# Optimization experiments

Measured on AMD Instinct MI355X. Metric: run time of the kernel, lower is better.

Reference implementation:

```python
import jax, jax.numpy as jnp
import numpy as np

B, D, H = 65536, 256, 16

def setup_inputs() -> dict:
    key = jax.random.key(0)
    k_x, k_w1, k_b1, k_w2, k_b2 = jax.random.split(key, 5)
    # per-feature subnet params: Linear(1,H) -> tanh -> Linear(H,1)
    # torch default init: U(-1/sqrt(fan_in), 1/sqrt(fan_in))
    w1 = jax.random.uniform(k_w1, (D, H), jnp.float32, -1.0, 1.0)          # fan_in=1
    b1 = jax.random.uniform(k_b1, (D, H), jnp.float32, -1.0, 1.0)
    bnd = 1.0 / np.sqrt(H)
    w2 = jax.random.uniform(k_w2, (D, H), jnp.float32, -bnd, bnd)          # fan_in=H
    b2 = jax.random.uniform(k_b2, (D,), jnp.float32, -bnd, bnd)
    x = jax.random.normal(k_x, (B, D), jnp.float32)
    return {"x": x, "w1": w1, "b1": b1, "w2": w2, "b2": b2}

def reference(x, w1, b1, w2, b2) -> jnp.ndarray:
    # h[b,d,h] = tanh(x[b,d]*w1[d,h] + b1[d,h])
    h = jnp.tanh(x[:, :, None] * w1[None, :, :] + b1[None, :, :])
    # out[b] = sum_d ( h[b,d,:] . w2[d,:] + b2[d] )
    out = jnp.einsum('bdh,dh->b', h, w2) + jnp.sum(b2)
    return out[:, None]  # [B, 1] to match torch output shape
```

## Files before the change

### kernel.cpp

```cpp
#include <hip/hip_runtime.h>
#include <hip/hip_fp16.h>
#include <cstdint>

#define B_TOT  65536
#define D_TOT  256
#define H_SUB  16

#define TBL_N      256
#define TBL_XMIN   (-8.0f)
#define TBL_DELTA  0.0625f
#define INV_DELTA  16.0f
#define T_OFF      128.0f

#define DG      32
#define NG      (D_TOT / DG)
#define RPB     512
#define NTH     256

__device__ __forceinline__ float tanh_fast(float z) {
    float e = __builtin_amdgcn_exp2f(z * 2.8853900817779268f);
    return 1.0f - 2.0f * __builtin_amdgcn_rcpf(e + 1.0f);
}

__global__ void build_tables(const float* __restrict__ w1,
                             const float* __restrict__ b1,
                             const float* __restrict__ w2,
                             const float* __restrict__ b2,
                             uint32_t* __restrict__ tab,
                             float* __restrict__ out) {
    int gid = blockIdx.x * NTH + threadIdx.x;
    out[gid] = 0.0f;
    int d = gid >> 8;
    int i = gid & (TBL_N - 1);
    float x0 = TBL_XMIN + (float)i * TBL_DELTA;
    float x1 = x0 + TBL_DELTA;
    float f0 = 0.0f, f1 = 0.0f;
#pragma unroll
    for (int h = 0; h < H_SUB; ++h) {
        float a = w1[d * H_SUB + h];
        float c = b1[d * H_SUB + h];
        float w = w2[d * H_SUB + h];
        f0 += w * tanh_fast(fmaf(a, x0, c));
        f1 += w * tanh_fast(fmaf(a, x1, c));
    }
    float val = f0 + b2[d];
    float slp = f1 - f0;
    __half2 h2 = __halves2half2(__float2half_rn(val), __float2half_rn(slp));
    tab[gid] = *reinterpret_cast<uint32_t*>(&h2);
}

__global__ __launch_bounds__(NTH, 4) void kan_forward(
        const float* __restrict__ x,
        const uint32_t* __restrict__ tab,
        float* __restrict__ out) {
    __shared__ uint32_t sT[DG * TBL_N];

    const int g  = blockIdx.x & (NG - 1);
    const int bc = blockIdx.x >> 3;

    {
        const uint4* src = reinterpret_cast<const uint4*>(tab + g * DG * TBL_N);
        uint4* dst = reinterpret_cast<uint4*>(sT);
#pragma unroll
        for (int k = 0; k < (DG * TBL_N / 4) / NTH; ++k)
            dst[threadIdx.x + k * NTH] = src[threadIdx.x + k * NTH];
    }
    __syncthreads();

    const int lane   = threadIdx.x & 63;
    const int wave   = threadIdx.x >> 6;
    const int subrow = lane >> 3;
    const int fq     = lane & 7;

    const int row0 = bc * RPB + wave * 8 + subrow;
    const float* xb = x + (size_t)row0 * D_TOT + g * DG + fq * 4;

#pragma unroll 4
    for (int it = 0; it < RPB / 32; ++it) {
        const float4 xv =
            *reinterpret_cast<const float4*>(xb + (size_t)it * 32 * D_TOT);
        float xs[4] = {xv.x, xv.y, xv.z, xv.w};
        float acc = 0.0f;
#pragma unroll
        for (int c = 0; c < 4; ++c) {
            float t = fmaf(xs[c], INV_DELTA, T_OFF);
            t = fminf(fmaxf(t, 0.0f), 255.99f);
            float fi = floorf(t);
            float u = t - fi;
            uint32_t e = sT[(fq * 4 + c) * TBL_N + (int)fi];
            union { uint32_t u32; __half2 h2; } cv;
            cv.u32 = e;
            acc += fmaf(__high2float(cv.h2), u, __low2float(cv.h2));
        }
        acc += __shfl_xor(acc, 1);
        acc += __shfl_xor(acc, 2);
        acc += __shfl_xor(acc, 4);
        if (fq == 0)
            atomicAdd(&out[row0 + it * 32], acc);
    }
}

extern "C" void kernel_launch(void* const* d_in, const int* in_sizes, int n_in,
                              void* d_out, int out_size, void* d_ws, size_t ws_size,
                              hipStream_t stream) {
    const float* x  = (const float*)d_in[0];
    const float* w1 = (const float*)d_in[1];
    const float* b1 = (const float*)d_in[2];
    const float* w2 = (const float*)d_in[3];
    const float* b2 = (const float*)d_in[4];
    float* out = (float*)d_out;
    uint32_t* tab = (uint32_t*)d_ws;

    build_tables<<<dim3(D_TOT * TBL_N / NTH), dim3(NTH), 0, stream>>>(
        w1, b1, w2, b2, tab, out);

    kan_forward<<<dim3((B_TOT / RPB) * NG), dim3(NTH), 0, stream>>>(
        x, tab, out);
}
```

Measured before the change: 109.1 us.

## Fuse table build and forward into one cooperative kernel with grid sync

Merges the table-building kernel and the forward kernel into a single cooperative launch. The first 256 blocks build the per-feature lookup tables and zero the output, then a grid-wide barrier runs before every block loads its table slice. Table building now evaluates the subnet once per grid point and takes slopes from shared memory, instead of evaluating it twice. This removes a second launch and its gap, but adds a grid-sync cost and requires all 1024 blocks to be co-resident.

```diff
diff --git a/kernel.cpp b/kernel.cpp
--- a/kernel.cpp
+++ b/kernel.cpp
@@ -1,5 +1,6 @@
 #include <hip/hip_runtime.h>
 #include <hip/hip_fp16.h>
+#include <hip/hip_cooperative_groups.h>
 #include <cstdint>
 
 #define B_TOT  65536
@@ -16,48 +17,64 @@
 #define NG      (D_TOT / DG)
 #define RPB     512
 #define NTH     256
+#define NBLK    ((B_TOT / RPB) * NG)
 
 __device__ __forceinline__ float tanh_fast(float z) {
     float e = __builtin_amdgcn_exp2f(z * 2.8853900817779268f);
     return 1.0f - 2.0f * __builtin_amdgcn_rcpf(e + 1.0f);
 }
 
-__global__ void build_tables(const float* __restrict__ w1,
-                             const float* __restrict__ b1,
-                             const float* __restrict__ w2,
-                             const float* __restrict__ b2,
-                             uint32_t* __restrict__ tab,
-                             float* __restrict__ out) {
-    int gid = blockIdx.x * NTH + threadIdx.x;
-    out[gid] = 0.0f;
-    int d = gid >> 8;
-    int i = gid & (TBL_N - 1);
-    float x0 = TBL_XMIN + (float)i * TBL_DELTA;
-    float x1 = x0 + TBL_DELTA;
-    float f0 = 0.0f, f1 = 0.0f;
-#pragma unroll
-    for (int h = 0; h < H_SUB; ++h) {
-        float a = w1[d * H_SUB + h];
-        float c = b1[d * H_SUB + h];
-        float w = w2[d * H_SUB + h];
-        f0 += w * tanh_fast(fmaf(a, x0, c));
-        f1 += w * tanh_fast(fmaf(a, x1, c));
-    }
-    float val = f0 + b2[d];
-    float slp = f1 - f0;
-    __half2 h2 = __halves2half2(__float2half_rn(val), __float2half_rn(slp));
-    tab[gid] = *reinterpret_cast<uint32_t*>(&h2);
-}
-
-__global__ __launch_bounds__(NTH, 4) void kan_forward(
+__global__ __launch_bounds__(NTH, 4) void kan_fused(
         const float* __restrict__ x,
-        const uint32_t* __restrict__ tab,
+        const float* __restrict__ w1,
+        const float* __restrict__ b1,
+        const float* __restrict__ w2,
+        const float* __restrict__ b2,
+        uint32_t* __restrict__ tab,
         float* __restrict__ out) {
     __shared__ uint32_t sT[DG * TBL_N];
+    float* sF = reinterpret_cast<float*>(sT);
+
+    if (blockIdx.x < D_TOT) {
+        const int d = blockIdx.x;
+        const int i = threadIdx.x;
+        out[d * NTH + i] = 0.0f;
+
+        float a[H_SUB], c[H_SUB], w[H_SUB];
+#pragma unroll
+        for (int h = 0; h < H_SUB; ++h) {
+            a[h] = w1[d * H_SUB + h];
+            c[h] = b1[d * H_SUB + h];
+            w[h] = w2[d * H_SUB + h];
+        }
+        float x0 = TBL_XMIN + (float)i * TBL_DELTA;
+        float f0 = 0.0f;
+#pragma unroll
+        for (int h = 0; h < H_SUB; ++h)
+            f0 += w[h] * tanh_fast(fmaf(a[h], x0, c[h]));
+        sF[i] = f0;
+        if (i == NTH - 1) {
+            float xe = TBL_XMIN + (float)TBL_N * TBL_DELTA;
+            float fe = 0.0f;
+#pragma unroll
+            for (int h = 0; h < H_SUB; ++h)
+                fe += w[h] * tanh_fast(fmaf(a[h], xe, c[h]));
+            sF[TBL_N] = fe;
+        }
+        __syncthreads();
+        float val = sF[i] + b2[d];
+        float slp = sF[i + 1] - sF[i];
+        __half2 h2 = __halves2half2(__float2half_rn(val), __float2half_rn(slp));
+        tab[d * TBL_N + i] = *reinterpret_cast<uint32_t*>(&h2);
+        __threadfence();
+    }
+
+    cooperative_groups::this_grid().sync();
 
     const int g  = blockIdx.x & (NG - 1);
     const int bc = blockIdx.x >> 3;
 
+    __syncthreads();
     {
         const uint4* src = reinterpret_cast<const uint4*>(tab + g * DG * TBL_N);
         uint4* dst = reinterpret_cast<uint4*>(sT);
@@ -82,12 +99,12 @@
         float xs[4] = {xv.x, xv.y, xv.z, xv.w};
         float acc = 0.0f;
 #pragma unroll
-        for (int c = 0; c < 4; ++c) {
-            float t = fmaf(xs[c], INV_DELTA, T_OFF);
+        for (int c2 = 0; c2 < 4; ++c2) {
+            float t = fmaf(xs[c2], INV_DELTA, T_OFF);
             t = fminf(fmaxf(t, 0.0f), 255.99f);
             float fi = floorf(t);
             float u = t - fi;
-            uint32_t e = sT[(fq * 4 + c) * TBL_N + (int)fi];
+            uint32_t e = sT[(fq * 4 + c2) * TBL_N + (int)fi];
             union { uint32_t u32; __half2 h2; } cv;
             cv.u32 = e;
             acc += fmaf(__high2float(cv.h2), u, __low2float(cv.h2));
@@ -111,9 +128,8 @@
     float* out = (float*)d_out;
     uint32_t* tab = (uint32_t*)d_ws;
 
-    build_tables<<<dim3(D_TOT * TBL_N / NTH), dim3(NTH), 0, stream>>>(
-        w1, b1, w2, b2, tab, out);
-
-    kan_forward<<<dim3((B_TOT / RPB) * NG), dim3(NTH), 0, stream>>>(
-        x, tab, out);
+    void* args[] = {(void*)&x, (void*)&w1, (void*)&b1, (void*)&w2,
+                    (void*)&b2, (void*)&tab, (void*)&out};
+    hipLaunchCooperativeKernel(reinterpret_cast<void*>(kan_fused),
+                               dim3(NBLK), dim3(NTH), args, 0, stream);
 }
```

After: 192.4 us. 1.76x slower.
